# Optimization experiments

Measured on AMD Instinct MI355X. Metric: run time of the kernel, lower is better.

The kernel has to match this reference:

```python
import jax, jax.numpy as jnp
import numpy as np

E = 262144          # number of atom pairs
NUM_PAIR_TYPES = 16 # num_type^2 = 4^2
DES_HIDDEN = 32
BASIS = 16
N_MAX = 8
BN_EPS = 1e-5


def _batchnorm1d(x, gamma, beta):
    # x: [E, C, 1]; torch BatchNorm1d normalizes per channel C over (N, L)
    mean = jnp.mean(x, axis=(0, 2), keepdims=True)
    var = jnp.var(x, axis=(0, 2), keepdims=True)  # biased, as torch BN
    xn = (x - mean) * jax.lax.rsqrt(var + BN_EPS)
    return xn * gamma[None, :, None] + beta[None, :, None]


def setup_inputs() -> dict:
    key = jax.random.key(0)
    k1, k2, k3, k4 = jax.random.split(key, 4)
    batch_ij = jax.random.randint(k1, (E,), 0, NUM_PAIR_TYPES, dtype=jnp.int32)
    batch_fn = jax.random.normal(k2, (E, BASIS, 1), dtype=jnp.float32)
    W0 = 0.1 * jax.random.normal(k3, (NUM_PAIR_TYPES, DES_HIDDEN, BASIS), dtype=jnp.float32)
    W1 = 0.1 * jax.random.normal(k4, (NUM_PAIR_TYPES, N_MAX, DES_HIDDEN), dtype=jnp.float32)
    return {
        "batch_ij": batch_ij,
        "batch_fn": batch_fn,
        "W0": W0,
        "W1": W1,
        "bn1_gamma": jnp.ones((DES_HIDDEN,), jnp.float32),
        "bn1_beta": jnp.zeros((DES_HIDDEN,), jnp.float32),
        "bn2_gamma": jnp.ones((N_MAX,), jnp.float32),
        "bn2_beta": jnp.zeros((N_MAX,), jnp.float32),
        "norm": 1,
    }


def reference(batch_ij, batch_fn, W0, W1, bn1_gamma, bn1_beta, bn2_gamma, bn2_beta, norm):
    # net_type == 'radial_hop' path
    # gather per-pair-type weights then batched matmul: [E,H,B] @ [E,B,1] -> [E,H,1]
    out = jnp.einsum('ehb,ebo->eho', W0[batch_ij], batch_fn)
    if norm:
        out = _batchnorm1d(out, bn1_gamma, bn1_beta)
    out = jax.nn.silu(out)
    # [E,N,H] @ [E,H,1] -> [E,N,1]
    out = jnp.einsum('enh,eho->eno', W1[batch_ij], out)
    if norm:
        out = _batchnorm1d(out, bn2_gamma, bn2_beta)
    out = jax.nn.silu(out)
    return out.reshape(-1, N_MAX)
```

## Files before the change

### kernel.cpp

```cpp
#include <hip/hip_runtime.h>

#define E_TOTAL 262144
#define TPB 512
#define NBLK 512
#define CHUNK 512
#define MAXT 48
#define W0R 24
#define W0T (32*W0R)
#define FNR 24
#define W1R 40
#define W1T (8*W1R)

typedef __attribute__((ext_vector_type(8))) short short8;
typedef __attribute__((ext_vector_type(4))) float f32x4;

__device__ __forceinline__ float silu_f(float x) { return x / (1.0f + __expf(-x)); }

__device__ __forceinline__ short f2bf(float f) {
    unsigned int u = __float_as_uint(f);
    u += 0x7fffu + ((u >> 16) & 1u);
    return (short)(u >> 16);
}
__device__ __forceinline__ float bf2f(short s) {
    return __uint_as_float(((unsigned int)(unsigned short)s) << 16);
}

template<int PHASE>
__global__ __launch_bounds__(TPB, 4)
void nep_main(const int* __restrict__ ij, const float* __restrict__ fn,
              const float* __restrict__ W0, const float* __restrict__ W1,
              const float* __restrict__ g1, const float* __restrict__ b1,
              const int* __restrict__ norm, const float* __restrict__ p1g,
              float* __restrict__ partial, short* __restrict__ o2b)
{
    __shared__ __align__(16) short sW0[16 * W0T];
    __shared__ __align__(16) short sW1[(PHASE == 1) ? 16 * W1T : 8];
    __shared__ __align__(16) short sfn[CHUNK * FNR];
    __shared__ int whist[8][16];
    __shared__ int woff[8][16];
    __shared__ int soff[16];
    __shared__ int tstart[17];
    __shared__ short slotp[MAXT * 16];
    __shared__ char ttype[MAXT];
    __shared__ float rS[8][32], rQ[8][32];
    __shared__ float fred[(PHASE == 1) ? 8 * 64 : 8];
    __shared__ float sAB1[64];

    const int tid  = threadIdx.x;
    const int bid  = blockIdx.x;
    const int l    = tid & 63;
    const int wave = tid >> 6;
    const int p    = l & 15;
    const int hi   = l >> 4;
    const int base = bid * CHUNK;

    const int t0 = ij[base + tid];
    const float4* f4g = (const float4*)(fn + (size_t)(base + tid) * 16);
    float4 u0 = f4g[0], u1 = f4g[1], u2 = f4g[2], u3 = f4g[3];

    unsigned long long bl0 = __ballot(t0 & 1);
    unsigned long long bl1 = __ballot(t0 & 2);
    unsigned long long bl2 = __ballot(t0 & 4);
    unsigned long long bl3 = __ballot(t0 & 8);
    unsigned long long mself = ((t0 & 1) ? bl0 : ~bl0) & ((t0 & 2) ? bl1 : ~bl1)
                             & ((t0 & 4) ? bl2 : ~bl2) & ((t0 & 8) ? bl3 : ~bl3);
    const int rank_w = __popcll(mself & ((1ull << l) - 1ull));
    if (l < 16) {
        const int t = l;
        unsigned long long mt = ((t & 1) ? bl0 : ~bl0) & ((t & 2) ? bl1 : ~bl1)
                              & ((t & 4) ? bl2 : ~bl2) & ((t & 8) ? bl3 : ~bl3);
        whist[wave][t] = __popcll(mt);
    }
    if (tid < MAXT * 16 / 2) ((int*)slotp)[tid] = -1;

    {
        const float4* W04 = (const float4*)W0;
        #pragma unroll
        for (int i = 0; i < 4; i++) {
            int g4 = tid + i * TPB;
            float4 v = W04[g4];
            int g = g4 * 4;
            int t = g >> 9, h = (g >> 4) & 31, k0 = g & 15;
            short4 s;
            s.x = f2bf(v.x); s.y = f2bf(v.y); s.z = f2bf(v.z); s.w = f2bf(v.w);
            *(short4*)(sW0 + t * W0T + h * W0R + k0) = s;
        }
    }
    if constexpr (PHASE == 1) {
        const float4* W14 = (const float4*)W1;
        #pragma unroll
        for (int i = 0; i < 2; i++) {
            int g4 = tid + i * TPB;
            float4 v = W14[g4];
            int g = g4 * 4;
            int t = g >> 8, n = (g >> 5) & 7, h0 = g & 31;
            short4 s;
            s.x = f2bf(v.x); s.y = f2bf(v.y); s.z = f2bf(v.z); s.w = f2bf(v.w);
            *(short4*)(sW1 + t * W1T + n * W1R + h0) = s;
        }
    }
    {
        short8 w0, w1;
        w0[0]=f2bf(u0.x); w0[1]=f2bf(u0.y); w0[2]=f2bf(u0.z); w0[3]=f2bf(u0.w);
        w0[4]=f2bf(u1.x); w0[5]=f2bf(u1.y); w0[6]=f2bf(u1.z); w0[7]=f2bf(u1.w);
        w1[0]=f2bf(u2.x); w1[1]=f2bf(u2.y); w1[2]=f2bf(u2.z); w1[3]=f2bf(u2.w);
        w1[4]=f2bf(u3.x); w1[5]=f2bf(u3.y); w1[6]=f2bf(u3.z); w1[7]=f2bf(u3.w);
        *(short8*)(sfn + tid * FNR)     = w0;
        *(short8*)(sfn + tid * FNR + 8) = w1;
    }
    if constexpr (PHASE == 1) {
        const int cc = tid & 63, j = tid >> 6;
        float s0 = 0.f, s1f = 0.f, s2f = 0.f, s3f = 0.f;
        #pragma unroll
        for (int m = 0; m < 16; m++) {
            s0  += p1g[(j + 8 * (4 * m + 0)) * 64 + cc];
            s1f += p1g[(j + 8 * (4 * m + 1)) * 64 + cc];
            s2f += p1g[(j + 8 * (4 * m + 2)) * 64 + cc];
            s3f += p1g[(j + 8 * (4 * m + 3)) * 64 + cc];
        }
        fred[j * 64 + cc] = (s0 + s1f) + (s2f + s3f);
    }
    __syncthreads();

    if (tid < 16) {
        int acc = 0;
        #pragma unroll
        for (int w = 0; w < 8; w++) { woff[w][tid] = acc; acc += whist[w][tid]; }
        soff[tid] = acc;
    }
    if constexpr (PHASE == 1) {
        if (tid < 64) {
            float st = 0.f;
            #pragma unroll
            for (int jj = 0; jj < 8; jj++) st += fred[jj * 64 + tid];
            fred[tid] = st;
        }
    }
    __syncthreads();
    if (tid < 16) {
        int nt = (soff[tid] + 15) >> 4;
        int inc = nt;
        #pragma unroll
        for (int off = 1; off < 16; off <<= 1) {
            int v = __shfl_up(inc, off, 64);
            if (tid >= off) inc += v;
        }
        tstart[tid] = inc - nt;
        if (tid == 15) tstart[16] = inc;
    }
    if constexpr (PHASE == 1) {
        if (tid >= 64 && tid < 96) {
            const int c = tid - 64;
            const float invE = 1.0f / (float)E_TOTAL;
            float mean = fred[c] * invE;
            float var  = fred[32 + c] * invE - mean * mean;
            float inv  = rsqrtf(var + 1e-5f);
            float a, b;
            if (*norm) { a = g1[c] * inv; b = b1[c] - mean * a; }
            else       { a = 1.f; b = 0.f; }
            sAB1[c]      = a;
            sAB1[32 + c] = b;
        }
    }
    __syncthreads();
    {
        const int rank = woff[wave][t0] + rank_w;
        const int ti = tstart[t0] + (rank >> 4);
        slotp[ti * 16 + (rank & 15)] = (short)tid;
        ttype[ti] = (char)t0;
    }
    __syncthreads();
    const int ntiles = tstart[16];

    float a1r[4], b1r[4], a1R[4], b1R[4];
    if constexpr (PHASE == 1) {
        #pragma unroll
        for (int r = 0; r < 4; r++) {
            a1r[r] = sAB1[hi * 4 + r];      b1r[r] = sAB1[32 + hi * 4 + r];
            a1R[r] = sAB1[16 + hi * 4 + r]; b1R[r] = sAB1[48 + hi * 4 + r];
        }
    }

    float s1[8], s2[8];
    #pragma unroll
    for (int c = 0; c < 8; c++) { s1[c] = 0.f; s2[c] = 0.f; }

    #pragma unroll 2
    for (int it = 0; it < 6; it++) {
        const int ti = wave + it * 8;
        const bool tv = (ti < ntiles);
        const int t  = tv ? (int)ttype[ti] : 0;
        const int sp = tv ? (int)slotp[ti * 16 + p] : -1;
        const bool vs = (sp >= 0);

        short8 bF = {0,0,0,0,0,0,0,0};
        if (hi < 2 && vs)
            bF = *(const short8*)(sfn + sp * FNR + hi * 8);
        const int hh = hi & 1;
        short8 a0 = *(const short8*)(sW0 + t * W0T + p * W0R + hh * 8);
        short8 a1 = *(const short8*)(sW0 + t * W0T + 16 * W0R + p * W0R + hh * 8);
        f32x4 z = {0.f, 0.f, 0.f, 0.f};
        f32x4 c0 = __builtin_amdgcn_mfma_f32_16x16x32_bf16(a0, bF, z, 0, 0, 0);
        f32x4 c1 = __builtin_amdgcn_mfma_f32_16x16x32_bf16(a1, bF, z, 0, 0, 0);

        if constexpr (PHASE == 0) {
            if (tv) {
                #pragma unroll
                for (int r = 0; r < 4; r++) {
                    s1[r]     += c0[r]; s2[r]     += c0[r] * c0[r];
                    s1[4 + r] += c1[r]; s2[4 + r] += c1[r] * c1[r];
                }
            }
        } else {
            short8 bS;
            #pragma unroll
            for (int r = 0; r < 4; r++) {
                float x0 = a1r[r] * c0[r] + b1r[r];
                float x1 = a1R[r] * c1[r] + b1R[r];
                bS[r]     = f2bf(vs ? silu_f(x0) : 0.f);
                bS[4 + r] = f2bf(vs ? silu_f(x1) : 0.f);
            }
            short8 a2v = {0,0,0,0,0,0,0,0};
            if (p < 8) {
                short4 A = *(const short4*)(sW1 + t * W1T + p * W1R + hi * 4);
                short4 B = *(const short4*)(sW1 + t * W1T + p * W1R + 16 + hi * 4);
                a2v[0] = A.x; a2v[1] = A.y; a2v[2] = A.z; a2v[3] = A.w;
                a2v[4] = B.x; a2v[5] = B.y; a2v[6] = B.z; a2v[7] = B.w;
            }
            f32x4 c2 = __builtin_amdgcn_mfma_f32_16x16x32_bf16(a2v, bS, z, 0, 0, 0);
            if (hi < 2 && vs) {
                short4 s;
                s.x = f2bf(c2[0]); s.y = f2bf(c2[1]); s.z = f2bf(c2[2]); s.w = f2bf(c2[3]);
                *(short4*)(o2b + (size_t)(base + sp) * 8 + hi * 4) = s;
            }
            if (tv) {
                #pragma unroll
                for (int r = 0; r < 4; r++) { s1[r] += c2[r]; s2[r] += c2[r] * c2[r]; }
            }
        }
    }

    constexpr int NC = (PHASE == 0) ? 8 : 4;
    #pragma unroll
    for (int c = 0; c < NC; c++) {
        float v1 = s1[c], v2 = s2[c];
        v1 += __shfl_xor(v1, 1, 64); v2 += __shfl_xor(v2, 1, 64);
        v1 += __shfl_xor(v1, 2, 64); v2 += __shfl_xor(v2, 2, 64);
        v1 += __shfl_xor(v1, 4, 64); v2 += __shfl_xor(v2, 4, 64);
        v1 += __shfl_xor(v1, 8, 64); v2 += __shfl_xor(v2, 8, 64);
        s1[c] = v1; s2[c] = v2;
    }
    if constexpr (PHASE == 0) {
        if (p == 0) {
            #pragma unroll
            for (int r = 0; r < 4; r++) {
                rS[wave][hi * 4 + r]      = s1[r];     rQ[wave][hi * 4 + r]      = s2[r];
                rS[wave][16 + hi * 4 + r] = s1[4 + r]; rQ[wave][16 + hi * 4 + r] = s2[4 + r];
            }
        }
        __syncthreads();
        if (tid < 32) {
            float a = 0.f, b = 0.f;
            #pragma unroll
            for (int w = 0; w < 8; w++) { a += rS[w][tid]; b += rQ[w][tid]; }
            partial[bid * 64 + tid]      = a;
            partial[bid * 64 + 32 + tid] = b;
        }
    } else {
        if (p == 0 && hi < 2) {
            #pragma unroll
            for (int r = 0; r < 4; r++) {
                rS[wave][hi * 4 + r] = s1[r];
                rQ[wave][hi * 4 + r] = s2[r];
            }
        }
        __syncthreads();
        if (tid < 8) {
            float a = 0.f, b = 0.f;
            #pragma unroll
            for (int w = 0; w < 8; w++) { a += rS[w][tid]; b += rQ[w][tid]; }
            partial[bid * 16 + tid]     = a;
            partial[bid * 16 + 8 + tid] = b;
        }
    }
}

__global__ __launch_bounds__(256)
void nep_bn2f(const short* __restrict__ o2b, const float* __restrict__ p2,
              const float* __restrict__ gamma, const float* __restrict__ beta,
              const int* __restrict__ norm, float* __restrict__ out)
{
    __shared__ float ssum[16][16];
    __shared__ float sA[8], sB[8];
    const int tid = threadIdx.x;
    {
        const int cc = tid & 15;
        const int j  = tid >> 4;
        float s = 0.f;
        for (int blk = j; blk < NBLK; blk += 16) s += p2[blk * 16 + cc];
        ssum[j][cc] = s;
    }
    __syncthreads();
    if (tid < 16) {
        float t = 0.f;
        #pragma unroll
        for (int jj = 0; jj < 16; jj++) t += ssum[jj][tid];
        ssum[0][tid] = t;
    }
    __syncthreads();
    if (tid < 8) {
        const float invE = 1.0f / (float)E_TOTAL;
        float mean = ssum[0][tid] * invE;
        float var  = ssum[0][8 + tid] * invE - mean * mean;
        float inv  = rsqrtf(var + 1e-5f);
        float a, b;
        if (*norm) { a = gamma[tid] * inv; b = beta[tid] - mean * a; }
        else       { a = 1.f; b = 0.f; }
        sA[tid] = a; sB[tid] = b;
    }
    __syncthreads();
    float a0 = sA[0], a1 = sA[1], a2 = sA[2], a3 = sA[3];
    float a4 = sA[4], a5 = sA[5], a6 = sA[6], a7 = sA[7];
    float b0 = sB[0], b1 = sB[1], b2 = sB[2], b3 = sB[3];
    float b4 = sB[4], b5 = sB[5], b6 = sB[6], b7 = sB[7];
    #pragma unroll
    for (int r = 0; r < 2; r++) {
        const int e = blockIdx.x * 256 + tid + r * (NBLK * 256);
        short8 v = *(const short8*)(o2b + (size_t)e * 8);
        float4 o0, o1;
        o0.x = silu_f(a0 * bf2f(v[0]) + b0);
        o0.y = silu_f(a1 * bf2f(v[1]) + b1);
        o0.z = silu_f(a2 * bf2f(v[2]) + b2);
        o0.w = silu_f(a3 * bf2f(v[3]) + b3);
        o1.x = silu_f(a4 * bf2f(v[4]) + b4);
        o1.y = silu_f(a5 * bf2f(v[5]) + b5);
        o1.z = silu_f(a6 * bf2f(v[6]) + b6);
        o1.w = silu_f(a7 * bf2f(v[7]) + b7);
        *(float4*)(out + (size_t)e * 8)     = o0;
        *(float4*)(out + (size_t)e * 8 + 4) = o1;
    }
}

extern "C" void kernel_launch(void* const* d_in, const int* in_sizes, int n_in,
                              void* d_out, int out_size, void* d_ws, size_t ws_size,
                              hipStream_t stream)
{
    const int*   ij   = (const int*)d_in[0];
    const float* fn   = (const float*)d_in[1];
    const float* W0   = (const float*)d_in[2];
    const float* W1   = (const float*)d_in[3];
    const float* g1   = (const float*)d_in[4];
    const float* b1   = (const float*)d_in[5];
    const float* g2   = (const float*)d_in[6];
    const float* b2   = (const float*)d_in[7];
    const int*   norm = (const int*)d_in[8];
    float* out = (float*)d_out;

    float* p1  = (float*)d_ws;
    float* p2  = p1 + NBLK * 64;
    short* o2b = (short*)(p2 + NBLK * 16);

    nep_main<0><<<NBLK, TPB, 0, stream>>>(ij, fn, W0, W1, g1, b1, norm, nullptr, p1, nullptr);
    nep_main<1><<<NBLK, TPB, 0, stream>>>(ij, fn, W0, W1, g1, b1, norm, p1, p2, o2b);
    nep_bn2f<<<NBLK, 256, 0, stream>>>(o2b, p2, g2, b2, norm, out);
}
```

Before: 41.15 us.

## Hoist weight loads early, vectorize partial reductions, halve bn2 grid

Global loads of W0 and W1 are issued at kernel start next to the fn loads, so their latency overlaps the ballot and histogram work. The phase-1 reduction of per-block BN1 partials now uses float4 loads across 32 row groups, with a wider second stage in shared memory. The final BN2+SiLU kernel launches 256 blocks that each process four elements per thread instead of two, and its partial-sum loop uses two accumulators. In exchange, register pressure rises and shared memory grows, which may lower occupancy.

```diff
diff --git a/kernel.cpp b/kernel.cpp
--- a/kernel.cpp
+++ b/kernel.cpp
@@ -10,6 +10,7 @@
 #define FNR 24
 #define W1R 40
 #define W1T (8*W1R)
+#define NBLK2 256
 
 typedef __attribute__((ext_vector_type(8))) short short8;
 typedef __attribute__((ext_vector_type(4))) float f32x4;
@@ -43,7 +44,7 @@
     __shared__ short slotp[MAXT * 16];
     __shared__ char ttype[MAXT];
     __shared__ float rS[8][32], rQ[8][32];
-    __shared__ float fred[(PHASE == 1) ? 8 * 64 : 8];
+    __shared__ float fred[(PHASE == 1) ? 32 * 64 : 8];
     __shared__ float sAB1[64];
 
     const int tid  = threadIdx.x;
@@ -57,6 +58,14 @@
     const int t0 = ij[base + tid];
     const float4* f4g = (const float4*)(fn + (size_t)(base + tid) * 16);
     float4 u0 = f4g[0], u1 = f4g[1], u2 = f4g[2], u3 = f4g[3];
+    const float4* W04 = (const float4*)W0;
+    float4 w0v0 = W04[tid],            w0v1 = W04[tid + TPB];
+    float4 w0v2 = W04[tid + 2 * TPB],  w0v3 = W04[tid + 3 * TPB];
+    float4 w1v0, w1v1;
+    if constexpr (PHASE == 1) {
+        const float4* W14 = (const float4*)W1;
+        w1v0 = W14[tid]; w1v1 = W14[tid + TPB];
+    }
 
     unsigned long long bl0 = __ballot(t0 & 1);
     unsigned long long bl1 = __ballot(t0 & 2);
@@ -74,12 +83,10 @@
     if (tid < MAXT * 16 / 2) ((int*)slotp)[tid] = -1;
 
     {
-        const float4* W04 = (const float4*)W0;
         #pragma unroll
         for (int i = 0; i < 4; i++) {
-            int g4 = tid + i * TPB;
-            float4 v = W04[g4];
-            int g = g4 * 4;
+            float4 v = (i == 0) ? w0v0 : (i == 1) ? w0v1 : (i == 2) ? w0v2 : w0v3;
+            int g = (tid + i * TPB) * 4;
             int t = g >> 9, h = (g >> 4) & 31, k0 = g & 15;
             short4 s;
             s.x = f2bf(v.x); s.y = f2bf(v.y); s.z = f2bf(v.z); s.w = f2bf(v.w);
@@ -87,12 +94,10 @@
         }
     }
     if constexpr (PHASE == 1) {
-        const float4* W14 = (const float4*)W1;
         #pragma unroll
         for (int i = 0; i < 2; i++) {
-            int g4 = tid + i * TPB;
-            float4 v = W14[g4];
-            int g = g4 * 4;
+            float4 v = (i == 0) ? w1v0 : w1v1;
+            int g = (tid + i * TPB) * 4;
             int t = g >> 8, n = (g >> 5) & 7, h0 = g & 31;
             short4 s;
             s.x = f2bf(v.x); s.y = f2bf(v.y); s.z = f2bf(v.z); s.w = f2bf(v.w);
@@ -109,16 +114,19 @@
         *(short8*)(sfn + tid * FNR + 8) = w1;
     }
     if constexpr (PHASE == 1) {
-        const int cc = tid & 63, j = tid >> 6;
-        float s0 = 0.f, s1f = 0.f, s2f = 0.f, s3f = 0.f;
-        #pragma unroll
-        for (int m = 0; m < 16; m++) {
-            s0  += p1g[(j + 8 * (4 * m + 0)) * 64 + cc];
-            s1f += p1g[(j + 8 * (4 * m + 1)) * 64 + cc];
-            s2f += p1g[(j + 8 * (4 * m + 2)) * 64 + cc];
-            s3f += p1g[(j + 8 * (4 * m + 3)) * 64 + cc];
-        }
-        fred[j * 64 + cc] = (s0 + s1f) + (s2f + s3f);
+        const int q = tid & 15;
+        const int j = tid >> 4;
+        float4 sa = {0.f,0.f,0.f,0.f}, sb = {0.f,0.f,0.f,0.f};
+        #pragma unroll
+        for (int m = 0; m < 16; m += 2) {
+            float4 a = *(const float4*)(p1g + (j + 32 * m) * 64 + q * 4);
+            float4 b = *(const float4*)(p1g + (j + 32 * (m + 1)) * 64 + q * 4);
+            sa.x += a.x; sa.y += a.y; sa.z += a.z; sa.w += a.w;
+            sb.x += b.x; sb.y += b.y; sb.z += b.z; sb.w += b.w;
+        }
+        float4 s;
+        s.x = sa.x + sb.x; s.y = sa.y + sb.y; s.z = sa.z + sb.z; s.w = sa.w + sb.w;
+        *(float4*)(fred + j * 64 + q * 4) = s;
     }
     __syncthreads();
 
@@ -129,11 +137,17 @@
         soff[tid] = acc;
     }
     if constexpr (PHASE == 1) {
-        if (tid < 64) {
-            float st = 0.f;
-            #pragma unroll
-            for (int jj = 0; jj < 8; jj++) st += fred[jj * 64 + tid];
-            fred[tid] = st;
+        if (tid >= 64 && tid < 128) {
+            const int c = tid - 64;
+            float q0 = 0.f, q1 = 0.f, q2 = 0.f, q3 = 0.f;
+            #pragma unroll
+            for (int jj = 0; jj < 32; jj += 4) {
+                q0 += fred[jj * 64 + c];
+                q1 += fred[(jj + 1) * 64 + c];
+                q2 += fred[(jj + 2) * 64 + c];
+                q3 += fred[(jj + 3) * 64 + c];
+            }
+            fred[c] = (q0 + q1) + (q2 + q3);
         }
     }
     __syncthreads();
@@ -149,8 +163,8 @@
         if (tid == 15) tstart[16] = inc;
     }
     if constexpr (PHASE == 1) {
-        if (tid >= 64 && tid < 96) {
-            const int c = tid - 64;
+        if (tid >= 128 && tid < 160) {
+            const int c = tid - 128;
             const float invE = 1.0f / (float)E_TOTAL;
             float mean = fred[c] * invE;
             float var  = fred[32 + c] * invE - mean * mean;
@@ -296,9 +310,12 @@
     {
         const int cc = tid & 15;
         const int j  = tid >> 4;
-        float s = 0.f;
-        for (int blk = j; blk < NBLK; blk += 16) s += p2[blk * 16 + cc];
-        ssum[j][cc] = s;
+        float q0 = 0.f, q1 = 0.f;
+        for (int blk = j; blk < NBLK; blk += 32) {
+            q0 += p2[blk * 16 + cc];
+            q1 += p2[(blk + 16) * 16 + cc];
+        }
+        ssum[j][cc] = q0 + q1;
     }
     __syncthreads();
     if (tid < 16) {
@@ -324,8 +341,8 @@
     float b0 = sB[0], b1 = sB[1], b2 = sB[2], b3 = sB[3];
     float b4 = sB[4], b5 = sB[5], b6 = sB[6], b7 = sB[7];
     #pragma unroll
-    for (int r = 0; r < 2; r++) {
-        const int e = blockIdx.x * 256 + tid + r * (NBLK * 256);
+    for (int r = 0; r < 4; r++) {
+        const int e = blockIdx.x * 256 + tid + r * (NBLK2 * 256);
         short8 v = *(const short8*)(o2b + (size_t)e * 8);
         float4 o0, o1;
         o0.x = silu_f(a0 * bf2f(v[0]) + b0);
@@ -362,5 +379,5 @@
 
     nep_main<0><<<NBLK, TPB, 0, stream>>>(ij, fn, W0, W1, g1, b1, norm, nullptr, p1, nullptr);
     nep_main<1><<<NBLK, TPB, 0, stream>>>(ij, fn, W0, W1, g1, b1, norm, p1, p2, o2b);
-    nep_bn2f<<<NBLK, 256, 0, stream>>>(o2b, p2, g2, b2, norm, out);
-}
+    nep_bn2f<<<NBLK2, 256, 0, stream>>>(o2b, p2, g2, b2, norm, out);
+}
```

After: 37.40 us (median of 2 runs). -9.1%, faster.
